# Kernel optimization log

Hardware: AMD Instinct MI355X
Metric: run time of the kernel (lower is better)

Reference implementation:

```python
import jax, jax.numpy as jnp
import numpy as np

NX, NY = 100, 100
FLOW_EXP = 1.25          # 5/4
K_SHEET = 0.01           # sheet_conductivity
K_CHAN = 0.1             # channel_conductivity
CAVITY_SPACING = 2.0
ICE_RHO, WATER_RHO, LATENT = 917.0, 1000.0, 3.34e5
DISS = (1.0 / ICE_RHO - 1.0 / WATER_RHO) / LATENT  # dissipation_coeff


def _build_grid(nx, ny):
    """Raster grid: degree-4 adjacency (E,W,N,S) with -1 padding, aligned link ids."""
    N = nx * ny
    xg, yg = np.meshgrid(np.arange(nx), np.arange(ny))
    x, y = xg.ravel(), yg.ravel()
    nid = y * nx + x
    nh = (nx - 1) * ny  # number of horizontal links
    adj = -np.ones((N, 4), np.int64)
    lnk = -np.ones((N, 4), np.int64)
    e = x < nx - 1
    adj[e, 0] = nid[e] + 1;  lnk[e, 0] = y[e] * (nx - 1) + x[e]
    w = x > 0
    adj[w, 1] = nid[w] - 1;  lnk[w, 1] = y[w] * (nx - 1) + x[w] - 1
    no = y < ny - 1
    adj[no, 2] = nid[no] + nx;  lnk[no, 2] = nh + y[no] * nx + x[no]
    so = y > 0
    adj[so, 3] = nid[so] - nx;  lnk[so, 3] = nh + (y[so] - 1) * nx + x[so]
    ids = np.arange(N).reshape(ny, nx)
    tail = np.concatenate([ids[:, :-1].ravel(), ids[:-1, :].ravel()])
    head = np.concatenate([ids[:, 1:].ravel(), ids[1:, :].ravel()])
    boundary = (x == 0) | (x == nx - 1) | (y == 0) | (y == ny - 1)
    inout = np.where(boundary, 1, -1).astype(np.int32)
    return (adj.astype(np.int32), lnk.astype(np.int32),
            head.astype(np.int32), tail.astype(np.int32), inout)


def setup_inputs() -> dict:
    key = jax.random.key(0)
    k = jax.random.split(key, 5)
    adj, lnk, head, tail, inout = _build_grid(NX, NY)
    N = NX * NY
    L = head.size
    pot = jax.random.normal(k[0], (N,), jnp.float32) * 1e4 + 1e6
    channel_size = jax.random.uniform(k[1], (L,), jnp.float32, 0.1, 2.0)
    sheet = jax.random.uniform(k[2], (N,), jnp.float32, 0.01, 0.5)
    face_len = jax.random.uniform(k[3], (L,), jnp.float32, 50.0, 150.0)
    link_len = jax.random.uniform(k[4], (L,), jnp.float32, 50.0, 150.0)
    return dict(previous_potential=pot, channel_size=channel_size,
                sheet_thickness=sheet, length_of_face=face_len,
                length_of_link=link_len,
                adjacent_nodes=jnp.asarray(adj), links_at_node=jnp.asarray(lnk),
                face_at_link=jnp.arange(L, dtype=jnp.int32),
                link_head=jnp.asarray(head), link_tail=jnp.asarray(tail),
                inflow_outflow=jnp.asarray(inout))


def reference(previous_potential, channel_size, sheet_thickness,
              length_of_face, length_of_link, adjacent_nodes, links_at_node,
              face_at_link, link_head, link_tail, inflow_outflow):
    N = previous_potential.shape[0]
    # --- link fields ---
    grad = (previous_potential[link_head] - previous_potential[link_tail]) / length_of_link  # [L]
    chan_q = -K_CHAN * channel_size ** FLOW_EXP * grad                                        # [L]
    st_link = 0.5 * (sheet_thickness[link_head] + sheet_thickness[link_tail])
    sheet_q = -K_SHEET * st_link ** FLOW_EXP * jnp.abs(grad) ** (-0.5) * grad                 # [L]
    # --- per (node, neighbor-slot) terms, [N,4] ---
    mask = adjacent_nodes != -1
    j = jnp.where(mask, adjacent_nodes, 0)
    lid = jnp.where(mask, links_at_node, 0)
    fl = length_of_face[face_at_link[lid]]
    ll = length_of_link[lid]
    i_idx = jnp.arange(N)[:, None]
    # NOTE: source indexes channel_size (a link field) by node id; reproduced faithfully.
    cs = 0.5 * (channel_size[i_idx] + channel_size[j])
    st = 0.5 * (sheet_thickness[i_idx] + sheet_thickness[j])
    g = grad[lid]
    sheet_flux = -K_SHEET * st ** FLOW_EXP * jnp.abs(g) ** (-0.5) * fl / ll
    chan_flux = -K_CHAN * cs ** FLOW_EXP * fl / ll
    ch_diss = jnp.abs(DISS * chan_q[lid] * fl)
    sh_diss = jnp.abs(DISS * sheet_q[lid] * CAVITY_SPACING * fl)
    term = jnp.where(mask, sheet_flux + chan_flux + ch_diss + sh_diss, 0.0)  # [N,4]
    # --- assemble dense operator ---
    M = jnp.zeros((N, N), previous_potential.dtype)
    rows = jnp.broadcast_to(i_idx, term.shape)
    M = M.at[rows, j].add(-term)                       # off-diagonal scatter
    M = M.at[jnp.arange(N), jnp.arange(N)].add(term.sum(axis=1))  # diagonal
    bnd = inflow_outflow == 1
    M = jnp.where(bnd[:, None], jnp.eye(N, dtype=M.dtype), M)     # Dirichlet rows
    return M
```

## Files before the change

kernel.cpp:

```cpp
#include <hip/hip_runtime.h>
#include <math.h>

#define K_SHEET   0.01f
#define K_CHAN    0.1f
#define CAV_SPACE 2.0f
#define FLOW_EXP  1.25f

__device__ __constant__ float c_diss = (float)((1.0 / 917.0 - 1.0 / 1000.0) / 3.34e5);

__global__ void sgds_patch_kernel(const float* __restrict__ pot,
                                  const float* __restrict__ chan,
                                  const float* __restrict__ sheet,
                                  const float* __restrict__ face_len,
                                  const float* __restrict__ link_len,
                                  const int*   __restrict__ adj,
                                  const int*   __restrict__ lnk,
                                  const int*   __restrict__ face_at_link,
                                  const int*   __restrict__ head,
                                  const int*   __restrict__ tail,
                                  const int*   __restrict__ inout,
                                  float*       __restrict__ M,
                                  int N)
{
    int i = blockIdx.x * blockDim.x + threadIdx.x;
    if (i >= N) return;

    float* row = M + (size_t)i * (size_t)N;

    if (inout[i] == 1) {
        row[i] = 1.0f;
        return;
    }

    float diag = 0.0f;

    #pragma unroll
    for (int s = 0; s < 4; ++s) {
        int j = adj[i * 4 + s];
        if (j < 0) continue;
        int lid = lnk[i * 4 + s];

        int   h  = head[lid];
        int   t  = tail[lid];
        float ll = link_len[lid];
        float g  = (pot[h] - pot[t]) / ll;

        float cq  = -K_CHAN * powf(chan[lid], FLOW_EXP) * g;
        float stl = 0.5f * (sheet[h] + sheet[t]);
        float ginv_sqrt = 1.0f / sqrtf(fabsf(g));
        float sq  = -K_SHEET * powf(stl, FLOW_EXP) * ginv_sqrt * g;

        float fl = face_len[face_at_link[lid]];
        float cs = 0.5f * (chan[i] + chan[j]);
        float st = 0.5f * (sheet[i] + sheet[j]);

        float sheet_flux = -K_SHEET * powf(st, FLOW_EXP) * ginv_sqrt * fl / ll;
        float chan_flux  = -K_CHAN  * powf(cs, FLOW_EXP) * fl / ll;
        float ch_diss    = fabsf(c_diss * cq * fl);
        float sh_diss    = fabsf(c_diss * sq * CAV_SPACE * fl);

        float term = sheet_flux + chan_flux + ch_diss + sh_diss;

        row[j] = -term;
        diag  += term;
    }

    row[i] = diag;
}

extern "C" void kernel_launch(void* const* d_in, const int* in_sizes, int n_in,
                              void* d_out, int out_size, void* d_ws, size_t ws_size,
                              hipStream_t stream) {
    const float* pot      = (const float*)d_in[0];
    const float* chan     = (const float*)d_in[1];
    const float* sheet    = (const float*)d_in[2];
    const float* face_len = (const float*)d_in[3];
    const float* link_len = (const float*)d_in[4];
    const int*   adj      = (const int*)d_in[5];
    const int*   lnk      = (const int*)d_in[6];
    const int*   fal      = (const int*)d_in[7];
    const int*   head     = (const int*)d_in[8];
    const int*   tail     = (const int*)d_in[9];
    const int*   inout    = (const int*)d_in[10];

    float* M = (float*)d_out;
    int N = in_sizes[0];

    hipMemsetAsync(d_out, 0, (size_t)out_size * sizeof(float), stream);

    int block = 256;
    int grid  = (N + block - 1) / block;
    sgds_patch_kernel<<<grid, block, 0, stream>>>(pot, chan, sheet, face_len, link_len,
                                                  adj, lnk, fal, head, tail, inout, M, N);
}
```

Before: 418.4 us.

## Fuse zero-fill into row-per-block kernel writing full rows with float4 stores

New measurement: 419.5 us. No clear change (+0.3%).

```diff
diff --git a/kernel.cpp b/kernel.cpp
--- a/kernel.cpp
+++ b/kernel.cpp
@@ -8,64 +8,104 @@
 
 __device__ __constant__ float c_diss = (float)((1.0 / 917.0 - 1.0 / 1000.0) / 3.34e5);
 
-__global__ void sgds_patch_kernel(const float* __restrict__ pot,
-                                  const float* __restrict__ chan,
-                                  const float* __restrict__ sheet,
-                                  const float* __restrict__ face_len,
-                                  const float* __restrict__ link_len,
-                                  const int*   __restrict__ adj,
-                                  const int*   __restrict__ lnk,
-                                  const int*   __restrict__ face_at_link,
-                                  const int*   __restrict__ head,
-                                  const int*   __restrict__ tail,
-                                  const int*   __restrict__ inout,
-                                  float*       __restrict__ M,
-                                  int N)
+__global__ __launch_bounds__(256)
+void sgds_row_kernel(const float* __restrict__ pot,
+                     const float* __restrict__ chan,
+                     const float* __restrict__ sheet,
+                     const float* __restrict__ face_len,
+                     const float* __restrict__ link_len,
+                     const int*   __restrict__ adj,
+                     const int*   __restrict__ lnk,
+                     const int*   __restrict__ fal,
+                     const int*   __restrict__ head,
+                     const int*   __restrict__ tail,
+                     const int*   __restrict__ inout,
+                     float*       __restrict__ M,
+                     int N)
 {
-    int i = blockIdx.x * blockDim.x + threadIdx.x;
-    if (i >= N) return;
+    const int i   = blockIdx.x;
+    const int tid = threadIdx.x;
 
-    float* row = M + (size_t)i * (size_t)N;
+    __shared__ float s_term[4];
+    __shared__ int   s_col[4];
 
-    if (inout[i] == 1) {
-        row[i] = 1.0f;
-        return;
+    const bool dirichlet = (inout[i] == 1);
+
+    if (!dirichlet && tid < 4) {
+        const int s = tid;
+        int j = adj[i * 4 + s];
+        if (j < 0) {
+            s_col[s] = -1;
+        } else {
+            int   lid = lnk[i * 4 + s];
+            int   h   = head[lid];
+            int   t   = tail[lid];
+            float ll  = link_len[lid];
+            float g   = (pot[h] - pot[t]) / ll;
+
+            float cq  = -K_CHAN * powf(chan[lid], FLOW_EXP) * g;
+            float stl = 0.5f * (sheet[h] + sheet[t]);
+            float ginv_sqrt = 1.0f / sqrtf(fabsf(g));
+            float sq  = -K_SHEET * powf(stl, FLOW_EXP) * ginv_sqrt * g;
+
+            float fl = face_len[fal[lid]];
+            float cs = 0.5f * (chan[i] + chan[j]);
+            float st = 0.5f * (sheet[i] + sheet[j]);
+
+            float sheet_flux = -K_SHEET * powf(st, FLOW_EXP) * ginv_sqrt * fl / ll;
+            float chan_flux  = -K_CHAN  * powf(cs, FLOW_EXP) * fl / ll;
+            float ch_diss    = fabsf(c_diss * cq * fl);
+            float sh_diss    = fabsf(c_diss * sq * CAV_SPACE * fl);
+
+            s_term[s] = sheet_flux + chan_flux + ch_diss + sh_diss;
+            s_col[s]  = j;
+        }
+    }
+    __syncthreads();
+
+    int   c0 = -1, c1 = -1, c2 = -1, c3 = -1;
+    float v0 = 0.f, v1 = 0.f, v2 = 0.f, v3 = 0.f;
+    float v4;
+    const int c4 = i;
+
+    if (dirichlet) {
+        v4 = 1.0f;
+    } else {
+        float diag = 0.0f;
+        if (s_col[0] >= 0) { c0 = s_col[0]; float t = s_term[0]; v0 = -t; diag += t; }
+        if (s_col[1] >= 0) { c1 = s_col[1]; float t = s_term[1]; v1 = -t; diag += t; }
+        if (s_col[2] >= 0) { c2 = s_col[2]; float t = s_term[2]; v2 = -t; diag += t; }
+        if (s_col[3] >= 0) { c3 = s_col[3]; float t = s_term[3]; v3 = -t; diag += t; }
+        v4 = diag;
     }
 
-    float diag = 0.0f;
+    int minc = c4, maxc = c4;
+    if (c0 >= 0) { minc = min(minc, c0); maxc = max(maxc, c0); }
+    if (c1 >= 0) { minc = min(minc, c1); maxc = max(maxc, c1); }
+    if (c2 >= 0) { minc = min(minc, c2); maxc = max(maxc, c2); }
+    if (c3 >= 0) { minc = min(minc, c3); maxc = max(maxc, c3); }
 
-    #pragma unroll
-    for (int s = 0; s < 4; ++s) {
-        int j = adj[i * 4 + s];
-        if (j < 0) continue;
-        int lid = lnk[i * 4 + s];
+    #define PICK(cc) ((cc) == c0 ? v0 : (cc) == c1 ? v1 : (cc) == c2 ? v2 : \
+                      (cc) == c3 ? v3 : (cc) == c4 ? v4 : 0.0f)
 
-        int   h  = head[lid];
-        int   t  = tail[lid];
-        float ll = link_len[lid];
-        float g  = (pot[h] - pot[t]) / ll;
+    float* __restrict__ row = M + (size_t)i * (size_t)N;
+    const int nvec = N >> 2;
 
-        float cq  = -K_CHAN * powf(chan[lid], FLOW_EXP) * g;
-        float stl = 0.5f * (sheet[h] + sheet[t]);
-        float ginv_sqrt = 1.0f / sqrtf(fabsf(g));
-        float sq  = -K_SHEET * powf(stl, FLOW_EXP) * ginv_sqrt * g;
-
-        float fl = face_len[face_at_link[lid]];
-        float cs = 0.5f * (chan[i] + chan[j]);
-        float st = 0.5f * (sheet[i] + sheet[j]);
-
-        float sheet_flux = -K_SHEET * powf(st, FLOW_EXP) * ginv_sqrt * fl / ll;
-        float chan_flux  = -K_CHAN  * powf(cs, FLOW_EXP) * fl / ll;
-        float ch_diss    = fabsf(c_diss * cq * fl);
-        float sh_diss    = fabsf(c_diss * sq * CAV_SPACE * fl);
-
-        float term = sheet_flux + chan_flux + ch_diss + sh_diss;
-
-        row[j] = -term;
-        diag  += term;
+    for (int v = tid; v < nvec; v += 256) {
+        int c = v << 2;
+        float4 out = make_float4(0.f, 0.f, 0.f, 0.f);
+        if (c <= maxc && c + 3 >= minc) {
+            out.x = PICK(c);
+            out.y = PICK(c + 1);
+            out.z = PICK(c + 2);
+            out.w = PICK(c + 3);
+        }
+        reinterpret_cast<float4*>(row)[v] = out;
     }
-
-    row[i] = diag;
+    for (int c = (nvec << 2) + tid; c < N; c += 256) {
+        row[c] = PICK(c);
+    }
+    #undef PICK
 }
 
 extern "C" void kernel_launch(void* const* d_in, const int* in_sizes, int n_in,
@@ -86,10 +126,6 @@
     float* M = (float*)d_out;
     int N = in_sizes[0];
 
-    hipMemsetAsync(d_out, 0, (size_t)out_size * sizeof(float), stream);
-
-    int block = 256;
-    int grid  = (N + block - 1) / block;
-    sgds_patch_kernel<<<grid, block, 0, stream>>>(pot, chan, sheet, face_len, link_len,
-                                                  adj, lnk, fal, head, tail, inout, M, N);
+    sgds_row_kernel<<<N, 256, 0, stream>>>(pot, chan, sheet, face_len, link_len,
+                                           adj, lnk, fal, head, tail, inout, M, N);
 }
```
